# Kernel optimization log

Measured on AMD Instinct MI355X. Metric: run time of the kernel, lower is better.

Reference implementation:

```python
import jax, jax.numpy as jnp
import numpy as np
import math

N = 4096
D = 256


def _xavier(key, shape):
    fan_in, fan_out = shape[0], shape[1]
    std = math.sqrt(2.0 / (fan_in + fan_out))
    return jax.random.normal(key, shape, dtype=jnp.float32) * std


def setup_inputs() -> dict:
    key = jax.random.key(0)
    ks = jax.random.split(key, 12)
    return {
        "cur": jax.random.normal(ks[0], (N, D), dtype=jnp.float32),
        "pre": jax.random.normal(ks[1], (N, D), dtype=jnp.float32),
        # SpatialHyperedge params
        "r_proj_s": _xavier(ks[2], (D, D)),
        "incidence_s": _xavier(ks[3], (N, N - 1)),
        # TemporalHyperedge params
        "r_proj_t": _xavier(ks[4], (D, D)),
        "incidence_t": _xavier(ks[5], (N, N)),
        # HHNodeMP params
        "node_proj": _xavier(ks[6], (D, D)),
        "spa_edge_proj": _xavier(ks[7], (D, D)),
        "tmp_edge_proj": _xavier(ks[8], (D, D)),
        "theta_w": _xavier(ks[9], (D, D)),
        "theta_b": jnp.zeros((D,), dtype=jnp.float32),
    }


def _scatter_slave(vals):
    """Place [N, N-1] per-row slave values into a zero-diagonal [N, N] matrix.
    Row i's k-th slave is column k if k < i else k+1 (all j != i in order)."""
    n = vals.shape[0]
    k = jnp.arange(n - 1)[None, :]
    cols = k + (k >= jnp.arange(n)[:, None])  # [N, N-1] column indices
    rows = jnp.broadcast_to(jnp.arange(n)[:, None], (n, n - 1))
    return jnp.zeros((n, n), dtype=vals.dtype).at[rows.reshape(-1), cols.reshape(-1)].set(vals.reshape(-1))


def _fro(x):
    return jnp.sqrt(jnp.sum(x * x))


def reference(cur, pre, r_proj_s, incidence_s, r_proj_t, incidence_t,
              node_proj, spa_edge_proj, tmp_edge_proj, theta_w, theta_b):
    n, d = cur.shape
    inv_sqrt_d = 1.0 / math.sqrt(d)

    # ---- SpatialHyperedge ----
    Xd = jax.lax.stop_gradient(cur)
    master_s = Xd @ r_proj_s                                   # [N, D]
    M_s_full = _scatter_slave(incidence_s)                     # [N, N], zero diag
    neigh_recon_s = M_s_full @ Xd                              # == bmm over gathered slaves
    spatial_loss = (_fro(master_s - neigh_recon_s) * 0.2
                    + jnp.sum(jnp.abs(incidence_s))
                    + 0.001 * _fro(incidence_s))
    # clamp(min=0) then zero-out entries not strictly > 0  => relu-like
    clipped_s = jnp.where(incidence_s > 0.0, incidence_s, 0.0)
    incidence_all = _scatter_slave(clipped_s) + jnp.eye(n, dtype=cur.dtype)

    # ---- TemporalHyperedge ----
    cur_d = jax.lax.stop_gradient(cur)
    pre_d = jax.lax.stop_gradient(pre)
    master_t = cur_d @ r_proj_t
    neigh_recon_t = incidence_t @ pre_d
    temporal_loss = (_fro(master_t - neigh_recon_t) * 0.2
                     + jnp.sum(jnp.abs(incidence_t))
                     + 0.001 * _fro(incidence_t))
    incidence_t_clipped = jnp.maximum(incidence_t, 0.0)

    # ---- SpatialHyperedgeMP ----
    spa_edge_fea = incidence_all @ cur
    spa_deg = jnp.sum(incidence_all, axis=1, keepdims=True)
    spa_emb = spa_edge_fea / spa_deg                           # [N, D]

    # ---- TemporalHyperedgeMP ----
    tmp_edge_fea = incidence_t_clipped @ pre + cur
    tmp_deg = jnp.sum(incidence_t_clipped, axis=1, keepdims=True) + 1.0
    tmp_emb = tmp_edge_fea / tmp_deg                           # [N, D]

    # ---- HHNodeMP ----
    node_fea = cur @ node_proj
    spa_fea = spa_emb @ spa_edge_proj
    tmp_fea = tmp_emb @ tmp_edge_proj
    spa_attn = jnp.sum(spa_fea * node_fea, axis=1, keepdims=True) * inv_sqrt_d
    tmp_attn = jnp.sum(tmp_fea * node_fea, axis=1, keepdims=True) * inv_sqrt_d
    val = spa_attn * spa_fea + tmp_attn * tmp_fea
    node_emb = jax.nn.relu(val @ theta_w.T + theta_b)          # dropout = identity (eval)

    return node_emb, temporal_loss + spatial_loss
```

## Files before the change

kernel.cpp:

```cpp
#include <hip/hip_runtime.h>
#include <hip/hip_bf16.h>
#include <math.h>

#define NN 4096
#define DD 256

typedef __bf16 bf16x8 __attribute__((ext_vector_type(8)));
typedef short  short8 __attribute__((ext_vector_type(8)));
typedef float  f32x4  __attribute__((ext_vector_type(4)));
typedef float  f32x16 __attribute__((ext_vector_type(16)));

typedef __attribute__((address_space(1))) const void gv_t;
typedef __attribute__((address_space(3))) void lv_t;
#define GLD16(gp, lp) __builtin_amdgcn_global_load_lds((gv_t*)(gp), (lv_t*)(lp), 16, 0, 0)

#define MFMA16(a, b, c) __builtin_amdgcn_mfma_f32_16x16x32_bf16((a), (b), (c), 0, 0, 0)
#define MFMA32(a, b, c) __builtin_amdgcn_mfma_f32_32x32x16_bf16((a), (b), (c), 0, 0, 0)

__device__ inline bf16x8 brelu(bf16x8 a) {
    short8 s = __builtin_bit_cast(short8, a);
    s = s & ~(s >> 15);
    return __builtin_bit_cast(bf16x8, s);
}

__device__ inline float wave_red(float v) {
#pragma unroll
    for (int o = 32; o > 0; o >>= 1) v += __shfl_down(v, o, 64);
    return v;
}

__device__ inline unsigned short bfbits(float f) {
    return __builtin_bit_cast(unsigned short, (__bf16)f);
}

__device__ inline void syncb() {
    asm volatile("s_waitcnt lgkmcnt(0)" ::: "memory");
    __builtin_amdgcn_s_barrier();
}

__device__ inline void store16(float* base, const f32x16& v, int lane) {
#pragma unroll
    for (int r4 = 0; r4 < 4; ++r4) {
        f32x4 c = {v[4 * r4], v[4 * r4 + 1], v[4 * r4 + 2], v[4 * r4 + 3]};
        ((f32x4*)base)[r4 * 64 + lane] = c;
    }
}
__device__ inline void add16(f32x16& v, const float* base, int lane) {
#pragma unroll
    for (int r4 = 0; r4 < 4; ++r4) {
        f32x4 c = ((const f32x4*)base)[r4 * 64 + lane];
        v[4 * r4] += c[0]; v[4 * r4 + 1] += c[1]; v[4 * r4 + 2] += c[2]; v[4 * r4 + 3] += c[3];
    }
}

template <int W>
__device__ inline void red_owner(f32x16 (&aR)[2][2], f32x16 (&aL)[2][2],
                                 float* scr, int lane, f32x16& oR, f32x16& oL) {
    constexpr int o1 = W ^ 1, o2 = W ^ 2, o3 = W ^ 3;
    store16(scr + W * 1024,       aR[o1 >> 1][o1 & 1], lane);
    store16(scr + (4 + W) * 1024, aR[o2 >> 1][o2 & 1], lane);
    syncb();
    oR = aR[W >> 1][W & 1];
    add16(oR, scr + o1 * 1024, lane);
    add16(oR, scr + (4 + o2) * 1024, lane);
    syncb();
    store16(scr + W * 1024, aR[o3 >> 1][o3 & 1], lane);
    syncb();
    add16(oR, scr + o3 * 1024, lane);
    syncb();
    store16(scr + W * 1024,       aL[o1 >> 1][o1 & 1], lane);
    store16(scr + (4 + W) * 1024, aL[o2 >> 1][o2 & 1], lane);
    syncb();
    oL = aL[W >> 1][W & 1];
    add16(oL, scr + o1 * 1024, lane);
    add16(oL, scr + (4 + o2) * 1024, lane);
    syncb();
    store16(scr + W * 1024, aL[o3 >> 1][o3 & 1], lane);
    syncb();
    add16(oL, scr + o3 * 1024, lane);
}

__global__ __launch_bounds__(256) void k_pre(
    const float* __restrict__ cur, const float* __restrict__ pre,
    const float* __restrict__ r_proj_s, const float* __restrict__ r_proj_t,
    const float* __restrict__ node_pj, const float* __restrict__ spa_pj,
    const float* __restrict__ tmp_pj, const float* __restrict__ theta_w,
    const float* __restrict__ inc_t, const float* __restrict__ inc_s,
    __bf16* __restrict__ cur_bf, __bf16* __restrict__ curT, __bf16* __restrict__ preT,
    __bf16* __restrict__ pTs, __bf16* __restrict__ pTt, __bf16* __restrict__ pTn,
    __bf16* __restrict__ pTspa, __bf16* __restrict__ pTtmp, __bf16* __restrict__ thetaBf,
    __bf16* __restrict__ Mt, __bf16* __restrict__ Ms,
    float* __restrict__ rsT, float* __restrict__ pAbsT, float* __restrict__ pSqT,
    float* __restrict__ rsS, float* __restrict__ pAbsS, float* __restrict__ pSqS) {
    __shared__ __align__(16) char psm[9280];
    const int b = blockIdx.x, t = threadIdx.x;
    if (b < 4096) {
        const int i = b;
        float (*red)[4] = (float (*)[4])psm;
        const float4* src = (const float4*)(inc_t + (size_t)i * NN);
        ushort4* dst = (ushort4*)(Mt + (size_t)i * NN);
        float rs = 0.f, as = 0.f, qs = 0.f;
#pragma unroll
        for (int e = 0; e < 4; ++e) {
            const int f = t + 256 * e;
            float4 v = src[f];
            float x[4] = {v.x, v.y, v.z, v.w};
            unsigned short o[4];
#pragma unroll
            for (int j = 0; j < 4; ++j) {
                float fv = x[j];
                as += fabsf(fv); qs += fv * fv; rs += fmaxf(fv, 0.f);
                o[j] = bfbits(fv);
            }
            dst[f] = make_ushort4(o[0], o[1], o[2], o[3]);
        }
        const int w = t >> 6, lane = t & 63;
        rs = wave_red(rs); as = wave_red(as); qs = wave_red(qs);
        if (lane == 0) { red[0][w] = rs; red[1][w] = as; red[2][w] = qs; }
        __syncthreads();
        if (t == 0) {
            rsT[i]   = red[0][0] + red[0][1] + red[0][2] + red[0][3];
            pAbsT[i] = red[1][0] + red[1][1] + red[1][2] + red[1][3];
            pSqT[i]  = red[2][0] + red[2][1] + red[2][2] + red[2][3];
        }
    } else if (b < 8192) {
        const int i = b - 4096;
        unsigned short* row = (unsigned short*)psm;
        float (*red)[4] = (float (*)[4])(psm + 8192);
        const float* srow = inc_s + (size_t)i * (NN - 1);
        float rs = 0.f, as = 0.f, qs = 0.f;
#pragma unroll
        for (int e = 0; e < 4; ++e) {
            const int f = t + 256 * e;
            float x[4] = {0.f, 0.f, 0.f, 0.f};
            if (f < 1023) __builtin_memcpy(x, srow + 4 * f, 16);
            else          __builtin_memcpy(x, srow + 4092, 12);
#pragma unroll
            for (int j = 0; j < 4; ++j) {
                const int k = 4 * f + j;
                float fv = x[j];
                as += fabsf(fv); qs += fv * fv; rs += fmaxf(fv, 0.f);
                if (k < NN - 1) row[k + (k >= i)] = bfbits(fv);
            }
        }
        if (t == 0) row[i] = 0;
        __syncthreads();
        uint4* dOut = (uint4*)(Ms + (size_t)i * NN);
        const uint4* sIn = (const uint4*)row;
        dOut[t] = sIn[t];
        dOut[t + 256] = sIn[t + 256];
        const int w = t >> 6, lane = t & 63;
        rs = wave_red(rs); as = wave_red(as); qs = wave_red(qs);
        if (lane == 0) { red[0][w] = rs; red[1][w] = as; red[2][w] = qs; }
        __syncthreads();
        if (t == 0) {
            rsS[i]   = red[0][0] + red[0][1] + red[0][2] + red[0][3];
            pAbsS[i] = red[1][0] + red[1][1] + red[1][2] + red[1][3];
            pSqS[i]  = red[2][0] + red[2][1] + red[2][2] + red[2][3];
        }
    } else if (b < 8704) {
        const int bb = b - 8192;
        const int x = bb & 63, y = (bb >> 6) & 3, z = bb >> 8;
        const int i0 = x * 64, d0 = y * 64;
        const float* src = z ? pre : cur;
        __bf16* dstT = z ? preT : curT;
        unsigned short (*tile)[72] = (unsigned short (*)[72])psm;
        const int r = t >> 2, c4 = (t & 3) * 16;
        const float* srow = src + (size_t)(i0 + r) * DD + d0 + c4;
        alignas(16) unsigned short loc[16];
#pragma unroll
        for (int e = 0; e < 4; ++e) {
            float4 v = ((const float4*)srow)[e];
            loc[e * 4 + 0] = bfbits(v.x);
            loc[e * 4 + 1] = bfbits(v.y);
            loc[e * 4 + 2] = bfbits(v.z);
            loc[e * 4 + 3] = bfbits(v.w);
        }
#pragma unroll
        for (int e = 0; e < 16; ++e) tile[r][c4 + e] = loc[e];
        if (z == 0) {
            __bf16* drow = cur_bf + (size_t)(i0 + r) * DD + d0 + c4;
            *(uint4*)drow = *(uint4*)&loc[0];
            *(uint4*)(drow + 8) = *(uint4*)&loc[8];
        }
        __syncthreads();
        alignas(16) unsigned short o[16];
#pragma unroll
        for (int e = 0; e < 16; ++e) o[e] = tile[c4 + e][r];
        __bf16* trow = dstT + (size_t)(d0 + r) * NN + i0 + c4;
        *(uint4*)trow = *(uint4*)&o[0];
        *(uint4*)(trow + 8) = *(uint4*)&o[8];
    } else {
        const int bb = b - 8704;
        const int id = bb >> 8, r = bb & 255;
        const float* src = id == 0 ? r_proj_s : id == 1 ? r_proj_t : id == 2 ? node_pj
                         : id == 3 ? spa_pj : id == 4 ? tmp_pj : theta_w;
        __bf16* dst = id == 0 ? pTs : id == 1 ? pTt : id == 2 ? pTn
                    : id == 3 ? pTspa : id == 4 ? pTtmp : thetaBf;
        float v = src[r * DD + t];
        if (id < 5) dst[t * DD + r] = (__bf16)v;
        else        dst[r * DD + t] = (__bf16)v;
    }
}

__device__ inline void mfma_step_s(const __bf16 (&As)[64][72], const __bf16 (&Bs)[64][72],
                                   int wr, int wc, int quad, int l16,
                                   f32x4 (&accR)[2][2]) {
#pragma unroll
    for (int ks = 0; ks < 2; ++ks) {
        const int kc = ks * 32 + quad * 8;
        bf16x8 a0 = *(const bf16x8*)&As[wr * 32 + l16][kc];
        bf16x8 a1 = *(const bf16x8*)&As[wr * 32 + 16 + l16][kc];
        bf16x8 b0 = *(const bf16x8*)&Bs[wc * 32 + l16][kc];
        bf16x8 b1 = *(const bf16x8*)&Bs[wc * 32 + 16 + l16][kc];
        accR[0][0] = MFMA16(a0, b0, accR[0][0]);
        accR[0][1] = MFMA16(a0, b1, accR[0][1]);
        accR[1][0] = MFMA16(a1, b0, accR[1][0]);
        accR[1][1] = MFMA16(a1, b1, accR[1][1]);
    }
}

__global__ __launch_bounds__(256, 2) void k_big(const __bf16* __restrict__ Mt, const __bf16* __restrict__ Ms,
                                                const __bf16* __restrict__ preT, const __bf16* __restrict__ curT,
                                                const float* __restrict__ negMt, const float* __restrict__ negMs,
                                                const float* __restrict__ cur,
                                                const float* __restrict__ rsT, const float* __restrict__ rsS,
                                                __bf16* __restrict__ embT, __bf16* __restrict__ embS,
                                                float* __restrict__ pDiff) {
    const int flat = blockIdx.x + 4 * (blockIdx.y + 64 * blockIdx.z);
    const int swz = (flat & 7) * 64 + (flat >> 3);
    const int bx = swz & 3, by = (swz >> 2) & 63, z = swz >> 8;
    const __bf16* A  = z ? Ms : Mt;
    const __bf16* BT = z ? curT : preT;
    const float* negM = z ? negMs : negMt;
    const float* rs   = z ? rsS : rsT;
    __bf16* emb       = z ? embS : embT;
    const int n0 = bx * 64, m0 = by * 64;
    __shared__ __align__(16) char smraw[65536];
    __bf16 (*sm)[2][64][64] = (__bf16 (*)[2][64][64])smraw;
    float* scr = (float*)smraw;
    f32x16 accR[2][2], accL[2][2];
#pragma unroll
    for (int i = 0; i < 2; ++i)
#pragma unroll
        for (int j = 0; j < 2; ++j) { accR[i][j] = (f32x16)0.f; accL[i][j] = (f32x16)0.f; }
    const int t = threadIdx.x, w = t >> 6, lane = t & 63;
    const int lr = lane >> 3, lc = lane & 7;
    const int q0 = 2 * w, q1 = q0 + 1;
    const int csw = (lc ^ lr) * 8;
    const __bf16* gA0 = A + (size_t)(m0 + 8 * q0 + lr) * NN + csw;
    const __bf16* gA1 = A + (size_t)(m0 + 8 * q1 + lr) * NN + csw;
    const __bf16* gB0 = BT + (size_t)(n0 + 8 * q0 + lr) * NN + csw;
    const __bf16* gB1 = BT + (size_t)(n0 + 8 * q1 + lr) * NN + csw;
    auto stage = [&](int b, int tk) {
        const int ko = tk * 64;
        GLD16(gA0 + ko, &sm[b][0][8 * q0][0]);
        GLD16(gA1 + ko, &sm[b][0][8 * q1][0]);
        GLD16(gB0 + ko, &sm[b][1][8 * q0][0]);
        GLD16(gB1 + ko, &sm[b][1][8 * q1][0]);
    };
    stage(0, 0); stage(1, 1); stage(2, 2); stage(3, 3);
    asm volatile("s_waitcnt vmcnt(8)" ::: "memory");
    __builtin_amdgcn_s_barrier();
    __builtin_amdgcn_sched_barrier(0);
    const int fr = lane & 31, h = lane >> 5;
    const int swc = ((2 * w + h) ^ (fr & 7)) * 8;
    for (int it = 0; it < 32; ++it) {
        const int b0 = (2 * it) & 3, b1 = b0 + 1;
        bf16x8 a[2][2], bb[2][2];
#pragma unroll
        for (int mi = 0; mi < 2; ++mi) {
            a[0][mi]  = *(const bf16x8*)&sm[b0][0][mi * 32 + fr][swc];
            a[1][mi]  = *(const bf16x8*)&sm[b1][0][mi * 32 + fr][swc];
            bb[0][mi] = *(const bf16x8*)&sm[b0][1][mi * 32 + fr][swc];
            bb[1][mi] = *(const bf16x8*)&sm[b1][1][mi * 32 + fr][swc];
        }
        asm volatile("s_waitcnt lgkmcnt(0)" ::: "memory");
        __builtin_amdgcn_sched_barrier(0);
        __builtin_amdgcn_s_barrier();
        __builtin_amdgcn_sched_barrier(0);
        if (it < 30) { stage(b0, 2 * it + 4); stage(b1, 2 * it + 5); }
        __builtin_amdgcn_sched_barrier(0);
        __builtin_amdgcn_s_setprio(1);
#pragma unroll
        for (int u = 0; u < 2; ++u)
#pragma unroll
            for (int mi = 0; mi < 2; ++mi) {
                bf16x8 ar = brelu(a[u][mi]);
#pragma unroll
                for (int ni = 0; ni < 2; ++ni) {
                    accR[mi][ni] = MFMA32(a[u][mi], bb[u][ni], accR[mi][ni]);
                    accL[mi][ni] = MFMA32(ar,       bb[u][ni], accL[mi][ni]);
                }
            }
        __builtin_amdgcn_s_setprio(0);
        if (it < 31) {
            if (it < 30) asm volatile("s_waitcnt vmcnt(8)" ::: "memory");
            else         asm volatile("s_waitcnt vmcnt(0)" ::: "memory");
            __builtin_amdgcn_s_barrier();
            __builtin_amdgcn_sched_barrier(0);
        }
    }
    f32x16 oR, oL;
    if      (w == 0) red_owner<0>(accR, accL, scr, lane, oR, oL);
    else if (w == 1) red_owner<1>(accR, accL, scr, lane, oR, oL);
    else if (w == 2) red_owner<2>(accR, accL, scr, lane, oR, oL);
    else             red_owner<3>(accR, accL, scr, lane, oR, oL);
    const int mi = w >> 1, ni = w & 1;
    float sumd = 0.f;
#pragma unroll
    for (int reg = 0; reg < 16; ++reg) {
        const int rr = (reg & 3) + 8 * (reg >> 2) + 4 * h;
        const int gr = m0 + mi * 32 + rr;
        const int gc = n0 + ni * 32 + fr;
        const size_t idx = (size_t)gr * DD + gc;
        float diff = oR[reg] + negM[idx];
        sumd += diff * diff;
        emb[idx] = (__bf16)((oL[reg] + cur[idx]) * (1.f / (rs[gr] + 1.f)));
    }
    sumd = wave_red(sumd);
    float* sredp = (float*)(smraw + 32768);
    if (lane == 0) sredp[w] = sumd;
    __syncthreads();
    if (t == 0)
        pDiff[z * 256 + by * 4 + bx] = sredp[0] + sredp[1] + sredp[2] + sredp[3];
}

__global__ __launch_bounds__(256) void k_small3(const __bf16* __restrict__ cur_bf,
                                                const __bf16* __restrict__ pTs, const __bf16* __restrict__ pTt,
                                                const __bf16* __restrict__ pTn,
                                                float* __restrict__ negMs, float* __restrict__ negMt,
                                                float* __restrict__ nodeFea) {
    const int z = blockIdx.z;
    const __bf16* BT = z == 0 ? pTs : (z == 1 ? pTt : pTn);
    const int n0 = blockIdx.x * 64, m0 = blockIdx.y * 64;
    __shared__ __bf16 As[64][72], Bs[64][72];
    f32x4 accR[2][2];
#pragma unroll
    for (int i = 0; i < 2; ++i)
#pragma unroll
        for (int j = 0; j < 2; ++j) accR[i][j] = (f32x4)0.f;
    const int t = threadIdx.x, w = t >> 6, lane = t & 63, quad = lane >> 4, l16 = lane & 15;
    const int wr = w >> 1, wc = w & 1;
    const int sr = t >> 2, sc = (t & 3) * 16;
    const __bf16* gA = cur_bf + (size_t)(m0 + sr) * DD + sc;
    const __bf16* gB = BT + (size_t)(n0 + sr) * DD + sc;
    for (int kt = 0; kt < DD / 64; ++kt) {
        uint4 av0 = *(const uint4*)(gA);
        uint4 av1 = *(const uint4*)(gA + 8);
        uint4 bv0 = *(const uint4*)(gB);
        uint4 bv1 = *(const uint4*)(gB + 8);
        __syncthreads();
        *(uint4*)&As[sr][sc] = av0; *(uint4*)&As[sr][sc + 8] = av1;
        *(uint4*)&Bs[sr][sc] = bv0; *(uint4*)&Bs[sr][sc + 8] = bv1;
        __syncthreads();
        mfma_step_s(As, Bs, wr, wc, quad, l16, accR);
        gA += 64; gB += 64;
    }
#pragma unroll
    for (int mi = 0; mi < 2; ++mi)
#pragma unroll
        for (int ni = 0; ni < 2; ++ni)
#pragma unroll
            for (int r = 0; r < 4; ++r) {
                int gr = m0 + wr * 32 + mi * 16 + quad * 4 + r;
                int gc = n0 + wc * 32 + ni * 16 + l16;
                size_t idx = (size_t)gr * DD + gc;
                float v = accR[mi][ni][r];
                if (z == 0) negMs[idx] = -v;
                else if (z == 1) negMt[idx] = -v;
                else nodeFea[idx] = v;
            }
}

__global__ __launch_bounds__(256) void k_fea(const __bf16* __restrict__ embS, const __bf16* __restrict__ embT,
                                             const __bf16* __restrict__ pTspa, const __bf16* __restrict__ pTtmp,
                                             const float* __restrict__ nodeF,
                                             float* __restrict__ spaF, float* __restrict__ tmpF,
                                             float* __restrict__ pSpa, float* __restrict__ pTmp) {
    const int z = blockIdx.z;
    const __bf16* Ae = z ? embT : embS;
    const __bf16* BT = z ? pTtmp : pTspa;
    float* outF = z ? tmpF : spaF;
    float* pOut = z ? pTmp : pSpa;
    const int n0 = blockIdx.x * 64, m0 = blockIdx.y * 64;
    __shared__ __bf16 As[64][72], Bs[64][72];
    f32x4 accR[2][2];
#pragma unroll
    for (int i = 0; i < 2; ++i)
#pragma unroll
        for (int j = 0; j < 2; ++j) accR[i][j] = (f32x4)0.f;
    const int t = threadIdx.x, w = t >> 6, lane = t & 63, quad = lane >> 4, l16 = lane & 15;
    const int wr = w >> 1, wc = w & 1;
    const int sr = t >> 2, sc = (t & 3) * 16;
    const __bf16* gA = Ae + (size_t)(m0 + sr) * DD + sc;
    const __bf16* gB = BT + (size_t)(n0 + sr) * DD + sc;
    for (int kt = 0; kt < DD / 64; ++kt) {
        uint4 av0 = *(const uint4*)(gA);
        uint4 av1 = *(const uint4*)(gA + 8);
        uint4 bv0 = *(const uint4*)(gB);
        uint4 bv1 = *(const uint4*)(gB + 8);
        __syncthreads();
        *(uint4*)&As[sr][sc] = av0; *(uint4*)&As[sr][sc + 8] = av1;
        *(uint4*)&Bs[sr][sc] = bv0; *(uint4*)&Bs[sr][sc + 8] = bv1;
        __syncthreads();
        mfma_step_s(As, Bs, wr, wc, quad, l16, accR);
        gA += 64; gB += 64;
    }
    const int slice = blockIdx.x * 2 + wc;
#pragma unroll
    for (int mi = 0; mi < 2; ++mi)
#pragma unroll
        for (int r = 0; r < 4; ++r) {
            const int gr = m0 + wr * 32 + mi * 16 + quad * 4 + r;
            float s = 0.f;
#pragma unroll
            for (int ni = 0; ni < 2; ++ni) {
                const int gc = n0 + wc * 32 + ni * 16 + l16;
                const size_t idx = (size_t)gr * DD + gc;
                const float v = accR[mi][ni][r];
                outF[idx] = v;
                s += v * nodeF[idx];
            }
            s += __shfl_xor(s, 1, 64);
            s += __shfl_xor(s, 2, 64);
            s += __shfl_xor(s, 4, 64);
            s += __shfl_xor(s, 8, 64);
            if (l16 == 0) pOut[(size_t)slice * NN + gr] = s;
        }
}

__global__ __launch_bounds__(256) void k_final(const float* __restrict__ spaF, const float* __restrict__ tmpF,
                                               const float* __restrict__ pSpa, const float* __restrict__ pTmp,
                                               const __bf16* __restrict__ thetaBf, const float* __restrict__ thetaB,
                                               const float* __restrict__ pAbsT, const float* __restrict__ pSqT,
                                               const float* __restrict__ pAbsS, const float* __restrict__ pSqS,
                                               const float* __restrict__ pDiff,
                                               float* __restrict__ out) {
    const int n0 = blockIdx.x * 64, m0 = blockIdx.y * 64;
    __shared__ __bf16 As[64][72], Bs[64][72];
    f32x4 accR[2][2];
#pragma unroll
    for (int i = 0; i < 2; ++i)
#pragma unroll
        for (int j = 0; j < 2; ++j) accR[i][j] = (f32x4)0.f;
    const int t = threadIdx.x, w = t >> 6, lane = t & 63, quad = lane >> 4, l16 = lane & 15;
    const int wr = w >> 1, wc = w & 1;
    const int sr = t >> 2, sc = (t & 3) * 16;
    const int row = m0 + sr;
    float sa = 0.f, ta = 0.f;
#pragma unroll
    for (int j = 0; j < 8; ++j) {
        sa += pSpa[(size_t)j * NN + row];
        ta += pTmp[(size_t)j * NN + row];
    }
    sa *= 0.0625f; ta *= 0.0625f;
    const float* gS = spaF + (size_t)row * DD + sc;
    const float* gT = tmpF + (size_t)row * DD + sc;
    const __bf16* gB = thetaBf + (size_t)(n0 + sr) * DD + sc;
    for (int kt = 0; kt < DD / 64; ++kt) {
        __bf16 tmp[16];
#pragma unroll
        for (int e4 = 0; e4 < 4; ++e4) {
            float4 vs = ((const float4*)gS)[e4];
            float4 vt = ((const float4*)gT)[e4];
            tmp[e4 * 4 + 0] = (__bf16)(sa * vs.x + ta * vt.x);
            tmp[e4 * 4 + 1] = (__bf16)(sa * vs.y + ta * vt.y);
            tmp[e4 * 4 + 2] = (__bf16)(sa * vs.z + ta * vt.z);
            tmp[e4 * 4 + 3] = (__bf16)(sa * vs.w + ta * vt.w);
        }
        uint4 bv0 = *(const uint4*)(gB);
        uint4 bv1 = *(const uint4*)(gB + 8);
        __syncthreads();
        *(uint4*)&As[sr][sc] = *(uint4*)&tmp[0]; *(uint4*)&As[sr][sc + 8] = *(uint4*)&tmp[8];
        *(uint4*)&Bs[sr][sc] = bv0; *(uint4*)&Bs[sr][sc + 8] = bv1;
        __syncthreads();
        mfma_step_s(As, Bs, wr, wc, quad, l16, accR);
        gS += 64; gT += 64; gB += 64;
    }
#pragma unroll
    for (int mi = 0; mi < 2; ++mi)
#pragma unroll
        for (int ni = 0; ni < 2; ++ni)
#pragma unroll
            for (int r = 0; r < 4; ++r) {
                int gr = m0 + wr * 32 + mi * 16 + quad * 4 + r;
                int gc = n0 + wc * 32 + ni * 16 + l16;
                float v = accR[mi][ni][r] + thetaB[gc];
                out[(size_t)gr * DD + gc] = fmaxf(v, 0.f);
            }
    if (blockIdx.x == 0 && blockIdx.y == 0) {
        float aT = 0.f, qT = 0.f, aS = 0.f, qS = 0.f;
#pragma unroll
        for (int j = 0; j < 16; ++j) {
            const int i = t + 256 * j;
            aT += pAbsT[i]; qT += pSqT[i]; aS += pAbsS[i]; qS += pSqS[i];
        }
        float dT = pDiff[t], dS = pDiff[256 + t];
        aT = wave_red(aT); qT = wave_red(qT); aS = wave_red(aS); qS = wave_red(qS);
        dT = wave_red(dT); dS = wave_red(dS);
        float (*red)[4] = (float (*)[4])As;
        if (lane == 0) { red[0][w] = aT; red[1][w] = qT; red[2][w] = aS; red[3][w] = qS; red[4][w] = dT; red[5][w] = dS; }
        __syncthreads();
        if (t == 0) {
            float s[6];
#pragma unroll
            for (int k = 0; k < 6; ++k) s[k] = red[k][0] + red[k][1] + red[k][2] + red[k][3];
            float l = s[0] + 0.001f * sqrtf(s[1]) + 0.2f * sqrtf(s[4])
                    + s[2] + 0.001f * sqrtf(s[3]) + 0.2f * sqrtf(s[5]);
            out[(size_t)NN * DD] = l;
        }
    }
}

extern "C" void kernel_launch(void* const* d_in, const int* in_sizes, int n_in,
                              void* d_out, int out_size, void* d_ws, size_t ws_size,
                              hipStream_t stream) {
    (void)in_sizes; (void)n_in; (void)out_size; (void)ws_size;
    const float* cur      = (const float*)d_in[0];
    const float* pre      = (const float*)d_in[1];
    const float* r_proj_s = (const float*)d_in[2];
    const float* inc_s    = (const float*)d_in[3];
    const float* r_proj_t = (const float*)d_in[4];
    const float* inc_t    = (const float*)d_in[5];
    const float* node_pj  = (const float*)d_in[6];
    const float* spa_pj   = (const float*)d_in[7];
    const float* tmp_pj   = (const float*)d_in[8];
    const float* theta_w  = (const float*)d_in[9];
    const float* theta_b  = (const float*)d_in[10];
    float* out = (float*)d_out;

    char* p = (char*)d_ws;
    auto alloc = [&](size_t bytes) -> void* {
        void* r = (void*)p;
        p += (bytes + 255) & ~(size_t)255;
        return r;
    };
    __bf16* Mt      = (__bf16*)alloc((size_t)NN * NN * 2);
    __bf16* Ms      = (__bf16*)alloc((size_t)NN * NN * 2);
    __bf16* cur_bf  = (__bf16*)alloc((size_t)NN * DD * 2);
    __bf16* curT    = (__bf16*)alloc((size_t)NN * DD * 2);
    __bf16* preT    = (__bf16*)alloc((size_t)NN * DD * 2);
    __bf16* pTs     = (__bf16*)alloc((size_t)DD * DD * 2);
    __bf16* pTt     = (__bf16*)alloc((size_t)DD * DD * 2);
    __bf16* pTn     = (__bf16*)alloc((size_t)DD * DD * 2);
    __bf16* pTspa   = (__bf16*)alloc((size_t)DD * DD * 2);
    __bf16* pTtmp   = (__bf16*)alloc((size_t)DD * DD * 2);
    __bf16* thetaBf = (__bf16*)alloc((size_t)DD * DD * 2);
    __bf16* embS    = (__bf16*)alloc((size_t)NN * DD * 2);
    __bf16* embT    = (__bf16*)alloc((size_t)NN * DD * 2);
    float* negMs    = (float*)alloc((size_t)NN * DD * 4);
    float* negMt    = (float*)alloc((size_t)NN * DD * 4);
    float* nodeFea  = (float*)alloc((size_t)NN * DD * 4);
    float* spaF     = (float*)alloc((size_t)NN * DD * 4);
    float* tmpF     = (float*)alloc((size_t)NN * DD * 4);
    float* rsS      = (float*)alloc((size_t)NN * 4);
    float* rsT      = (float*)alloc((size_t)NN * 4);
    float* pSpa     = (float*)alloc((size_t)8 * NN * 4);
    float* pTmp     = (float*)alloc((size_t)8 * NN * 4);
    float* pAbsT    = (float*)alloc((size_t)NN * 4);
    float* pSqT     = (float*)alloc((size_t)NN * 4);
    float* pAbsS    = (float*)alloc((size_t)NN * 4);
    float* pSqS     = (float*)alloc((size_t)NN * 4);
    float* pDiff    = (float*)alloc(512 * 4);

    k_pre<<<10240, 256, 0, stream>>>(cur, pre, r_proj_s, r_proj_t, node_pj, spa_pj, tmp_pj, theta_w,
                                     inc_t, inc_s,
                                     cur_bf, curT, preT, pTs, pTt, pTn, pTspa, pTtmp, thetaBf,
                                     Mt, Ms, rsT, pAbsT, pSqT, rsS, pAbsS, pSqS);
    k_small3<<<dim3(4, 64, 3), 256, 0, stream>>>(cur_bf, pTs, pTt, pTn, negMs, negMt, nodeFea);
    k_big<<<dim3(4, 64, 2), 256, 0, stream>>>(Mt, Ms, preT, curT, negMt, negMs, cur,
                                              rsT, rsS, embT, embS, pDiff);
    k_fea<<<dim3(4, 64, 2), 256, 0, stream>>>(embS, embT, pTspa, pTtmp, nodeFea,
                                              spaF, tmpF, pSpa, pTmp);
    k_final<<<dim3(4, 64), 256, 0, stream>>>(spaF, tmpF, pSpa, pTmp, thetaBf, theta_b,
                                             pAbsT, pSqT, pAbsS, pSqS, pDiff, out);
}
```

Measured before the change: 243.7 us.

## Fuse incidence fp32-to-bf16 conversion and row stats into the big GEMM

The big GEMM kernel now reads the fp32 incidence matrices directly, converts them to bf16 in registers, and writes them into swizzled LDS. Row sums, abs sums and squared sums are accumulated in the same pass, so the separate pre-pass that wrote two 32MB bf16 matrices plus per-row stats is gone. This removes a full write and re-read of the converted matrices. In exchange the GEMM loads twice the bytes for A, and each of the four column blocks re-reads and re-converts the same rows. The spatial path also does scalar gathered loads to handle the skipped diagonal.

```diff
diff --git a/kernel.cpp b/kernel.cpp
--- a/kernel.cpp
+++ b/kernel.cpp
@@ -85,86 +85,16 @@
     const float* __restrict__ r_proj_s, const float* __restrict__ r_proj_t,
     const float* __restrict__ node_pj, const float* __restrict__ spa_pj,
     const float* __restrict__ tmp_pj, const float* __restrict__ theta_w,
-    const float* __restrict__ inc_t, const float* __restrict__ inc_s,
     __bf16* __restrict__ cur_bf, __bf16* __restrict__ curT, __bf16* __restrict__ preT,
     __bf16* __restrict__ pTs, __bf16* __restrict__ pTt, __bf16* __restrict__ pTn,
-    __bf16* __restrict__ pTspa, __bf16* __restrict__ pTtmp, __bf16* __restrict__ thetaBf,
-    __bf16* __restrict__ Mt, __bf16* __restrict__ Ms,
-    float* __restrict__ rsT, float* __restrict__ pAbsT, float* __restrict__ pSqT,
-    float* __restrict__ rsS, float* __restrict__ pAbsS, float* __restrict__ pSqS) {
-    __shared__ __align__(16) char psm[9280];
+    __bf16* __restrict__ pTspa, __bf16* __restrict__ pTtmp, __bf16* __restrict__ thetaBf) {
+    __shared__ unsigned short tile[64][72];
     const int b = blockIdx.x, t = threadIdx.x;
-    if (b < 4096) {
-        const int i = b;
-        float (*red)[4] = (float (*)[4])psm;
-        const float4* src = (const float4*)(inc_t + (size_t)i * NN);
-        ushort4* dst = (ushort4*)(Mt + (size_t)i * NN);
-        float rs = 0.f, as = 0.f, qs = 0.f;
-#pragma unroll
-        for (int e = 0; e < 4; ++e) {
-            const int f = t + 256 * e;
-            float4 v = src[f];
-            float x[4] = {v.x, v.y, v.z, v.w};
-            unsigned short o[4];
-#pragma unroll
-            for (int j = 0; j < 4; ++j) {
-                float fv = x[j];
-                as += fabsf(fv); qs += fv * fv; rs += fmaxf(fv, 0.f);
-                o[j] = bfbits(fv);
-            }
-            dst[f] = make_ushort4(o[0], o[1], o[2], o[3]);
-        }
-        const int w = t >> 6, lane = t & 63;
-        rs = wave_red(rs); as = wave_red(as); qs = wave_red(qs);
-        if (lane == 0) { red[0][w] = rs; red[1][w] = as; red[2][w] = qs; }
-        __syncthreads();
-        if (t == 0) {
-            rsT[i]   = red[0][0] + red[0][1] + red[0][2] + red[0][3];
-            pAbsT[i] = red[1][0] + red[1][1] + red[1][2] + red[1][3];
-            pSqT[i]  = red[2][0] + red[2][1] + red[2][2] + red[2][3];
-        }
-    } else if (b < 8192) {
-        const int i = b - 4096;
-        unsigned short* row = (unsigned short*)psm;
-        float (*red)[4] = (float (*)[4])(psm + 8192);
-        const float* srow = inc_s + (size_t)i * (NN - 1);
-        float rs = 0.f, as = 0.f, qs = 0.f;
-#pragma unroll
-        for (int e = 0; e < 4; ++e) {
-            const int f = t + 256 * e;
-            float x[4] = {0.f, 0.f, 0.f, 0.f};
-            if (f < 1023) __builtin_memcpy(x, srow + 4 * f, 16);
-            else          __builtin_memcpy(x, srow + 4092, 12);
-#pragma unroll
-            for (int j = 0; j < 4; ++j) {
-                const int k = 4 * f + j;
-                float fv = x[j];
-                as += fabsf(fv); qs += fv * fv; rs += fmaxf(fv, 0.f);
-                if (k < NN - 1) row[k + (k >= i)] = bfbits(fv);
-            }
-        }
-        if (t == 0) row[i] = 0;
-        __syncthreads();
-        uint4* dOut = (uint4*)(Ms + (size_t)i * NN);
-        const uint4* sIn = (const uint4*)row;
-        dOut[t] = sIn[t];
-        dOut[t + 256] = sIn[t + 256];
-        const int w = t >> 6, lane = t & 63;
-        rs = wave_red(rs); as = wave_red(as); qs = wave_red(qs);
-        if (lane == 0) { red[0][w] = rs; red[1][w] = as; red[2][w] = qs; }
-        __syncthreads();
-        if (t == 0) {
-            rsS[i]   = red[0][0] + red[0][1] + red[0][2] + red[0][3];
-            pAbsS[i] = red[1][0] + red[1][1] + red[1][2] + red[1][3];
-            pSqS[i]  = red[2][0] + red[2][1] + red[2][2] + red[2][3];
-        }
-    } else if (b < 8704) {
-        const int bb = b - 8192;
-        const int x = bb & 63, y = (bb >> 6) & 3, z = bb >> 8;
+    if (b < 512) {
+        const int x = b & 63, y = (b >> 6) & 3, z = b >> 8;
         const int i0 = x * 64, d0 = y * 64;
         const float* src = z ? pre : cur;
         __bf16* dstT = z ? preT : curT;
-        unsigned short (*tile)[72] = (unsigned short (*)[72])psm;
         const int r = t >> 2, c4 = (t & 3) * 16;
         const float* srow = src + (size_t)(i0 + r) * DD + d0 + c4;
         alignas(16) unsigned short loc[16];
@@ -191,7 +121,7 @@
         *(uint4*)trow = *(uint4*)&o[0];
         *(uint4*)(trow + 8) = *(uint4*)&o[8];
     } else {
-        const int bb = b - 8704;
+        const int bb = b - 512;
         const int id = bb >> 8, r = bb & 255;
         const float* src = id == 0 ? r_proj_s : id == 1 ? r_proj_t : id == 2 ? node_pj
                          : id == 3 ? spa_pj : id == 4 ? tmp_pj : theta_w;
@@ -201,6 +131,224 @@
         if (id < 5) dst[t * DD + r] = (__bf16)v;
         else        dst[r * DD + t] = (__bf16)v;
     }
+}
+
+template <int ZS>
+__device__ inline void loadApair(float (&x)[32], const float* rowp, int i, int kt0, int sc16) {
+#pragma unroll
+    for (int u = 0; u < 2; ++u) {
+        const int c0 = (kt0 + u) * 64 + sc16;
+        if (ZS == 0) {
+#pragma unroll
+            for (int j4 = 0; j4 < 4; ++j4) {
+                float4 v = *(const float4*)(rowp + c0 + 4 * j4);
+                x[u * 16 + 4 * j4 + 0] = v.x;
+                x[u * 16 + 4 * j4 + 1] = v.y;
+                x[u * 16 + 4 * j4 + 2] = v.z;
+                x[u * 16 + 4 * j4 + 3] = v.w;
+            }
+        } else {
+#pragma unroll
+            for (int j = 0; j < 16; ++j) {
+                const int k = c0 + j;
+                const int dg = (k == i);
+                int idx = dg ? 0 : (k - (k > i));
+                float v = rowp[idx];
+                x[u * 16 + j] = dg ? 0.f : v;
+            }
+        }
+    }
+}
+
+__device__ inline void writeApair(const float (&x)[32], __bf16 (*A0)[64], __bf16 (*A1)[64],
+                                  int sr, int pc0, int pc1,
+                                  float& rs, float& as, float& qs) {
+#pragma unroll
+    for (int u = 0; u < 2; ++u) {
+        __bf16 (*Ab)[64] = u ? A1 : A0;
+        alignas(16) unsigned short o[16];
+#pragma unroll
+        for (int j = 0; j < 16; ++j) {
+            float fv = x[u * 16 + j];
+            as += fabsf(fv); qs += fv * fv; rs += fmaxf(fv, 0.f);
+            o[j] = bfbits(fv);
+        }
+        *(uint4*)&Ab[sr][pc0] = *(uint4*)&o[0];
+        *(uint4*)&Ab[sr][pc1] = *(uint4*)&o[8];
+    }
+}
+
+template <int ZS>
+__device__ inline void iter_body(int P, float (&x)[32],
+                                 __bf16 (*A0)[64], __bf16 (*A1)[64],
+                                 __bf16 (*B0)[64], __bf16 (*B1)[64],
+                                 const float* rowp, int i, int sc16, int sr, int pc0, int pc1,
+                                 const __bf16* gB0, const __bf16* gB1,
+                                 __bf16* dB0a, __bf16* dB0b, __bf16* dB1a, __bf16* dB1b,
+                                 int fr, int swc,
+                                 f32x16 (&accR)[2][2], f32x16 (&accL)[2][2],
+                                 float& rs, float& as, float& qs) {
+    bf16x8 a[2][2], bb[2][2];
+#pragma unroll
+    for (int mi = 0; mi < 2; ++mi) {
+        a[0][mi]  = *(const bf16x8*)&A0[mi * 32 + fr][swc];
+        a[1][mi]  = *(const bf16x8*)&A1[mi * 32 + fr][swc];
+        bb[0][mi] = *(const bf16x8*)&B0[mi * 32 + fr][swc];
+        bb[1][mi] = *(const bf16x8*)&B1[mi * 32 + fr][swc];
+    }
+    asm volatile("s_waitcnt lgkmcnt(0)" ::: "memory");
+    __builtin_amdgcn_sched_barrier(0);
+    __builtin_amdgcn_s_barrier();
+    __builtin_amdgcn_sched_barrier(0);
+    __builtin_amdgcn_s_setprio(1);
+#pragma unroll
+    for (int u = 0; u < 2; ++u)
+#pragma unroll
+        for (int mi = 0; mi < 2; ++mi) {
+            bf16x8 ar = brelu(a[u][mi]);
+#pragma unroll
+            for (int ni = 0; ni < 2; ++ni) {
+                accR[mi][ni] = MFMA32(a[u][mi], bb[u][ni], accR[mi][ni]);
+                accL[mi][ni] = MFMA32(ar,       bb[u][ni], accL[mi][ni]);
+            }
+        }
+    __builtin_amdgcn_s_setprio(0);
+    __builtin_amdgcn_sched_barrier(0);
+    if (P < 29) {
+        if (ZS) asm volatile("s_waitcnt vmcnt(32)" ::: "memory");
+        else    asm volatile("s_waitcnt vmcnt(8)"  ::: "memory");
+    } else {
+        asm volatile("s_waitcnt vmcnt(0)" ::: "memory");
+    }
+    __builtin_amdgcn_sched_barrier(0);
+    if (P < 30) {
+        writeApair(x, A0, A1, sr, pc0, pc1, rs, as, qs);
+        const size_t tb = (size_t)(2 * (P + 2)) * 64;
+        GLD16(gB0 + tb, dB0a);      GLD16(gB1 + tb, dB0b);
+        GLD16(gB0 + tb + 64, dB1a); GLD16(gB1 + tb + 64, dB1b);
+    }
+    __builtin_amdgcn_sched_barrier(0);
+    if (P < 28) loadApair<ZS>(x, rowp, i, 2 * (P + 4), sc16);
+    asm volatile("s_waitcnt lgkmcnt(0)" ::: "memory");
+    __builtin_amdgcn_sched_barrier(0);
+    __builtin_amdgcn_s_barrier();
+}
+
+template <int ZS>
+__device__ inline void run_loop(const float* rowp, int i, const __bf16* BT, int n0, int t,
+                                char* smraw,
+                                f32x16 (&accR)[2][2], f32x16 (&accL)[2][2],
+                                float& rs, float& as, float& qs) {
+    __bf16 (*As)[64][64] = (__bf16 (*)[64][64])smraw;
+    __bf16 (*Bs)[64][64] = (__bf16 (*)[64][64])(smraw + 32768);
+    const int w = t >> 6, lane = t & 63;
+    const int sr = t >> 2, c4 = t & 3, sc16 = c4 * 16;
+    const int lr = lane >> 3, lc = lane & 7;
+    const int q0 = 2 * w, q1 = q0 + 1;
+    const int csw = (lc ^ lr) * 8;
+    const __bf16* gB0 = BT + (size_t)(n0 + 8 * q0 + lr) * NN + csw;
+    const __bf16* gB1 = BT + (size_t)(n0 + 8 * q1 + lr) * NN + csw;
+    const int fr = lane & 31, h = lane >> 5;
+    const int swc = ((2 * w + h) ^ (fr & 7)) * 8;
+    const int pc0 = ((2 * c4) ^ (sr & 7)) * 8;
+    const int pc1 = ((2 * c4 + 1) ^ (sr & 7)) * 8;
+    float x0[32], x1[32];
+    loadApair<ZS>(x0, rowp, i, 0, sc16);
+    loadApair<ZS>(x1, rowp, i, 2, sc16);
+    GLD16(gB0, &Bs[0][8 * q0][0]);            GLD16(gB1, &Bs[0][8 * q1][0]);
+    GLD16(gB0 + 64, &Bs[1][8 * q0][0]);       GLD16(gB1 + 64, &Bs[1][8 * q1][0]);
+    GLD16(gB0 + 128, &Bs[2][8 * q0][0]);      GLD16(gB1 + 128, &Bs[2][8 * q1][0]);
+    GLD16(gB0 + 192, &Bs[3][8 * q0][0]);      GLD16(gB1 + 192, &Bs[3][8 * q1][0]);
+    asm volatile("s_waitcnt vmcnt(0)" ::: "memory");
+    __builtin_amdgcn_sched_barrier(0);
+    writeApair(x0, As[0], As[1], sr, pc0, pc1, rs, as, qs);
+    writeApair(x1, As[2], As[3], sr, pc0, pc1, rs, as, qs);
+    __builtin_amdgcn_sched_barrier(0);
+    loadApair<ZS>(x0, rowp, i, 4, sc16);
+    loadApair<ZS>(x1, rowp, i, 6, sc16);
+    asm volatile("s_waitcnt lgkmcnt(0)" ::: "memory");
+    __builtin_amdgcn_sched_barrier(0);
+    __builtin_amdgcn_s_barrier();
+    for (int q = 0; q < 16; ++q) {
+        iter_body<ZS>(2 * q, x0, As[0], As[1], Bs[0], Bs[1], rowp, i, sc16, sr, pc0, pc1,
+                      gB0, gB1, &Bs[0][8 * q0][0], &Bs[0][8 * q1][0],
+                      &Bs[1][8 * q0][0], &Bs[1][8 * q1][0], fr, swc, accR, accL, rs, as, qs);
+        iter_body<ZS>(2 * q + 1, x1, As[2], As[3], Bs[2], Bs[3], rowp, i, sc16, sr, pc0, pc1,
+                      gB0, gB1, &Bs[2][8 * q0][0], &Bs[2][8 * q1][0],
+                      &Bs[3][8 * q0][0], &Bs[3][8 * q1][0], fr, swc, accR, accL, rs, as, qs);
+    }
+}
+
+__global__ __launch_bounds__(256, 2) void k_big(const float* __restrict__ inc_t,
+                                                const float* __restrict__ inc_s,
+                                                const __bf16* __restrict__ preT,
+                                                const __bf16* __restrict__ curT,
+                                                const float* __restrict__ negMt,
+                                                const float* __restrict__ negMs,
+                                                const float* __restrict__ cur,
+                                                __bf16* __restrict__ embT, __bf16* __restrict__ embS,
+                                                float* __restrict__ pDiff,
+                                                float* __restrict__ pAbs2, float* __restrict__ pSq2) {
+    const int flat = blockIdx.x + 4 * (blockIdx.y + 64 * blockIdx.z);
+    const int swz = (flat & 7) * 64 + (flat >> 3);
+    const int bx = swz & 3, by = (swz >> 2) & 63, z = swz >> 8;
+    const __bf16* BT  = z ? curT : preT;
+    const float* negM = z ? negMs : negMt;
+    __bf16* emb       = z ? embS : embT;
+    const int n0 = bx * 64, m0 = by * 64;
+    __shared__ __align__(16) char smraw[65536];
+    f32x16 accR[2][2], accL[2][2];
+#pragma unroll
+    for (int i = 0; i < 2; ++i)
+#pragma unroll
+        for (int j = 0; j < 2; ++j) { accR[i][j] = (f32x16)0.f; accL[i][j] = (f32x16)0.f; }
+    const int t = threadIdx.x, w = t >> 6, lane = t & 63;
+    const int sr = t >> 2;
+    const int gi = m0 + sr;
+    float rs = 0.f, as = 0.f, qs = 0.f;
+    if (z == 0) {
+        run_loop<0>(inc_t + (size_t)gi * NN, gi, BT, n0, t, smraw, accR, accL, rs, as, qs);
+    } else {
+        run_loop<1>(inc_s + (size_t)gi * (NN - 1), gi, BT, n0, t, smraw, accR, accL, rs, as, qs);
+    }
+    rs += __shfl_xor(rs, 1, 64);
+    rs += __shfl_xor(rs, 2, 64);
+    float* rs_lds = (float*)(smraw + 32768);
+    float (*red2)[4] = (float (*)[4])(smraw + 32768 + 256);
+    float* sredp = (float*)(smraw + 32768 + 304);
+    if ((t & 3) == 0) rs_lds[sr] = rs;
+    as = wave_red(as); qs = wave_red(qs);
+    if (lane == 0) { red2[0][w] = as; red2[1][w] = qs; }
+    __syncthreads();
+    if (bx == 0 && t == 0) {
+        pAbs2[z * 64 + by] = red2[0][0] + red2[0][1] + red2[0][2] + red2[0][3];
+        pSq2 [z * 64 + by] = red2[1][0] + red2[1][1] + red2[1][2] + red2[1][3];
+    }
+    float* scr = (float*)smraw;
+    f32x16 oR, oL;
+    if      (w == 0) red_owner<0>(accR, accL, scr, lane, oR, oL);
+    else if (w == 1) red_owner<1>(accR, accL, scr, lane, oR, oL);
+    else if (w == 2) red_owner<2>(accR, accL, scr, lane, oR, oL);
+    else             red_owner<3>(accR, accL, scr, lane, oR, oL);
+    const int mi = w >> 1, ni = w & 1;
+    const int fr = lane & 31, h = lane >> 5;
+    float sumd = 0.f;
+#pragma unroll
+    for (int reg = 0; reg < 16; ++reg) {
+        const int rr = (reg & 3) + 8 * (reg >> 2) + 4 * h;
+        const int gr = m0 + mi * 32 + rr;
+        const int gc = n0 + ni * 32 + fr;
+        const size_t idx = (size_t)gr * DD + gc;
+        float diff = oR[reg] + negM[idx];
+        sumd += diff * diff;
+        float inv = 1.f / (rs_lds[gr - m0] + 1.f);
+        emb[idx] = (__bf16)((oL[reg] + cur[idx]) * inv);
+    }
+    sumd = wave_red(sumd);
+    if (lane == 0) sredp[w] = sumd;
+    __syncthreads();
+    if (t == 0)
+        pDiff[z * 256 + by * 4 + bx] = sredp[0] + sredp[1] + sredp[2] + sredp[3];
 }
 
 __device__ inline void mfma_step_s(const __bf16 (&As)[64][72], const __bf16 (&Bs)[64][72],
@@ -218,112 +366,6 @@
         accR[1][0] = MFMA16(a1, b0, accR[1][0]);
         accR[1][1] = MFMA16(a1, b1, accR[1][1]);
     }
-}
-
-__global__ __launch_bounds__(256, 2) void k_big(const __bf16* __restrict__ Mt, const __bf16* __restrict__ Ms,
-                                                const __bf16* __restrict__ preT, const __bf16* __restrict__ curT,
-                                                const float* __restrict__ negMt, const float* __restrict__ negMs,
-                                                const float* __restrict__ cur,
-                                                const float* __restrict__ rsT, const float* __restrict__ rsS,
-                                                __bf16* __restrict__ embT, __bf16* __restrict__ embS,
-                                                float* __restrict__ pDiff) {
-    const int flat = blockIdx.x + 4 * (blockIdx.y + 64 * blockIdx.z);
-    const int swz = (flat & 7) * 64 + (flat >> 3);
-    const int bx = swz & 3, by = (swz >> 2) & 63, z = swz >> 8;
-    const __bf16* A  = z ? Ms : Mt;
-    const __bf16* BT = z ? curT : preT;
-    const float* negM = z ? negMs : negMt;
-    const float* rs   = z ? rsS : rsT;
-    __bf16* emb       = z ? embS : embT;
-    const int n0 = bx * 64, m0 = by * 64;
-    __shared__ __align__(16) char smraw[65536];
-    __bf16 (*sm)[2][64][64] = (__bf16 (*)[2][64][64])smraw;
-    float* scr = (float*)smraw;
-    f32x16 accR[2][2], accL[2][2];
-#pragma unroll
-    for (int i = 0; i < 2; ++i)
-#pragma unroll
-        for (int j = 0; j < 2; ++j) { accR[i][j] = (f32x16)0.f; accL[i][j] = (f32x16)0.f; }
-    const int t = threadIdx.x, w = t >> 6, lane = t & 63;
-    const int lr = lane >> 3, lc = lane & 7;
-    const int q0 = 2 * w, q1 = q0 + 1;
-    const int csw = (lc ^ lr) * 8;
-    const __bf16* gA0 = A + (size_t)(m0 + 8 * q0 + lr) * NN + csw;
-    const __bf16* gA1 = A + (size_t)(m0 + 8 * q1 + lr) * NN + csw;
-    const __bf16* gB0 = BT + (size_t)(n0 + 8 * q0 + lr) * NN + csw;
-    const __bf16* gB1 = BT + (size_t)(n0 + 8 * q1 + lr) * NN + csw;
-    auto stage = [&](int b, int tk) {
-        const int ko = tk * 64;
-        GLD16(gA0 + ko, &sm[b][0][8 * q0][0]);
-        GLD16(gA1 + ko, &sm[b][0][8 * q1][0]);
-        GLD16(gB0 + ko, &sm[b][1][8 * q0][0]);
-        GLD16(gB1 + ko, &sm[b][1][8 * q1][0]);
-    };
-    stage(0, 0); stage(1, 1); stage(2, 2); stage(3, 3);
-    asm volatile("s_waitcnt vmcnt(8)" ::: "memory");
-    __builtin_amdgcn_s_barrier();
-    __builtin_amdgcn_sched_barrier(0);
-    const int fr = lane & 31, h = lane >> 5;
-    const int swc = ((2 * w + h) ^ (fr & 7)) * 8;
-    for (int it = 0; it < 32; ++it) {
-        const int b0 = (2 * it) & 3, b1 = b0 + 1;
-        bf16x8 a[2][2], bb[2][2];
-#pragma unroll
-        for (int mi = 0; mi < 2; ++mi) {
-            a[0][mi]  = *(const bf16x8*)&sm[b0][0][mi * 32 + fr][swc];
-            a[1][mi]  = *(const bf16x8*)&sm[b1][0][mi * 32 + fr][swc];
-            bb[0][mi] = *(const bf16x8*)&sm[b0][1][mi * 32 + fr][swc];
-            bb[1][mi] = *(const bf16x8*)&sm[b1][1][mi * 32 + fr][swc];
-        }
-        asm volatile("s_waitcnt lgkmcnt(0)" ::: "memory");
-        __builtin_amdgcn_sched_barrier(0);
-        __builtin_amdgcn_s_barrier();
-        __builtin_amdgcn_sched_barrier(0);
-        if (it < 30) { stage(b0, 2 * it + 4); stage(b1, 2 * it + 5); }
-        __builtin_amdgcn_sched_barrier(0);
-        __builtin_amdgcn_s_setprio(1);
-#pragma unroll
-        for (int u = 0; u < 2; ++u)
-#pragma unroll
-            for (int mi = 0; mi < 2; ++mi) {
-                bf16x8 ar = brelu(a[u][mi]);
-#pragma unroll
-                for (int ni = 0; ni < 2; ++ni) {
-                    accR[mi][ni] = MFMA32(a[u][mi], bb[u][ni], accR[mi][ni]);
-                    accL[mi][ni] = MFMA32(ar,       bb[u][ni], accL[mi][ni]);
-                }
-            }
-        __builtin_amdgcn_s_setprio(0);
-        if (it < 31) {
-            if (it < 30) asm volatile("s_waitcnt vmcnt(8)" ::: "memory");
-            else         asm volatile("s_waitcnt vmcnt(0)" ::: "memory");
-            __builtin_amdgcn_s_barrier();
-            __builtin_amdgcn_sched_barrier(0);
-        }
-    }
-    f32x16 oR, oL;
-    if      (w == 0) red_owner<0>(accR, accL, scr, lane, oR, oL);
-    else if (w == 1) red_owner<1>(accR, accL, scr, lane, oR, oL);
-    else if (w == 2) red_owner<2>(accR, accL, scr, lane, oR, oL);
-    else             red_owner<3>(accR, accL, scr, lane, oR, oL);
-    const int mi = w >> 1, ni = w & 1;
-    float sumd = 0.f;
-#pragma unroll
-    for (int reg = 0; reg < 16; ++reg) {
-        const int rr = (reg & 3) + 8 * (reg >> 2) + 4 * h;
-        const int gr = m0 + mi * 32 + rr;
-        const int gc = n0 + ni * 32 + fr;
-        const size_t idx = (size_t)gr * DD + gc;
-        float diff = oR[reg] + negM[idx];
-        sumd += diff * diff;
-        emb[idx] = (__bf16)((oL[reg] + cur[idx]) * (1.f / (rs[gr] + 1.f)));
-    }
-    sumd = wave_red(sumd);
-    float* sredp = (float*)(smraw + 32768);
-    if (lane == 0) sredp[w] = sumd;
-    __syncthreads();
-    if (t == 0)
-        pDiff[z * 256 + by * 4 + bx] = sredp[0] + sredp[1] + sredp[2] + sredp[3];
 }
 
 __global__ __launch_bounds__(256) void k_small3(const __bf16* __restrict__ cur_bf,
@@ -433,8 +475,7 @@
 __global__ __launch_bounds__(256) void k_final(const float* __restrict__ spaF, const float* __restrict__ tmpF,
                                                const float* __restrict__ pSpa, const float* __restrict__ pTmp,
                                                const __bf16* __restrict__ thetaBf, const float* __restrict__ thetaB,
-                                               const float* __restrict__ pAbsT, const float* __restrict__ pSqT,
-                                               const float* __restrict__ pAbsS, const float* __restrict__ pSqS,
+                                               const float* __restrict__ pAbs2, const float* __restrict__ pSq2,
                                                const float* __restrict__ pDiff,
                                                float* __restrict__ out) {
     const int n0 = blockIdx.x * 64, m0 = blockIdx.y * 64;
@@ -491,11 +532,7 @@
             }
     if (blockIdx.x == 0 && blockIdx.y == 0) {
         float aT = 0.f, qT = 0.f, aS = 0.f, qS = 0.f;
-#pragma unroll
-        for (int j = 0; j < 16; ++j) {
-            const int i = t + 256 * j;
-            aT += pAbsT[i]; qT += pSqT[i]; aS += pAbsS[i]; qS += pSqS[i];
-        }
+        if (t < 64) { aT = pAbs2[t]; qT = pSq2[t]; aS = pAbs2[64 + t]; qS = pSq2[64 + t]; }
         float dT = pDiff[t], dS = pDiff[256 + t];
         aT = wave_red(aT); qT = wave_red(qT); aS = wave_red(aS); qS = wave_red(qS);
         dT = wave_red(dT); dS = wave_red(dS);
@@ -536,8 +573,6 @@
         p += (bytes + 255) & ~(size_t)255;
         return r;
     };
-    __bf16* Mt      = (__bf16*)alloc((size_t)NN * NN * 2);
-    __bf16* Ms      = (__bf16*)alloc((size_t)NN * NN * 2);
     __bf16* cur_bf  = (__bf16*)alloc((size_t)NN * DD * 2);
     __bf16* curT    = (__bf16*)alloc((size_t)NN * DD * 2);
     __bf16* preT    = (__bf16*)alloc((size_t)NN * DD * 2);
@@ -554,25 +589,19 @@
     float* nodeFea  = (float*)alloc((size_t)NN * DD * 4);
     float* spaF     = (float*)alloc((size_t)NN * DD * 4);
     float* tmpF     = (float*)alloc((size_t)NN * DD * 4);
-    float* rsS      = (float*)alloc((size_t)NN * 4);
-    float* rsT      = (float*)alloc((size_t)NN * 4);
     float* pSpa     = (float*)alloc((size_t)8 * NN * 4);
     float* pTmp     = (float*)alloc((size_t)8 * NN * 4);
-    float* pAbsT    = (float*)alloc((size_t)NN * 4);
-    float* pSqT     = (float*)alloc((size_t)NN * 4);
-    float* pAbsS    = (float*)alloc((size_t)NN * 4);
-    float* pSqS     = (float*)alloc((size_t)NN * 4);
+    float* pAbs2    = (float*)alloc(128 * 4);
+    float* pSq2     = (float*)alloc(128 * 4);
     float* pDiff    = (float*)alloc(512 * 4);
 
-    k_pre<<<10240, 256, 0, stream>>>(cur, pre, r_proj_s, r_proj_t, node_pj, spa_pj, tmp_pj, theta_w,
-                                     inc_t, inc_s,
-                                     cur_bf, curT, preT, pTs, pTt, pTn, pTspa, pTtmp, thetaBf,
-                                     Mt, Ms, rsT, pAbsT, pSqT, rsS, pAbsS, pSqS);
+    k_pre<<<2048, 256, 0, stream>>>(cur, pre, r_proj_s, r_proj_t, node_pj, spa_pj, tmp_pj, theta_w,
+                                    cur_bf, curT, preT, pTs, pTt, pTn, pTspa, pTtmp, thetaBf);
     k_small3<<<dim3(4, 64, 3), 256, 0, stream>>>(cur_bf, pTs, pTt, pTn, negMs, negMt, nodeFea);
-    k_big<<<dim3(4, 64, 2), 256, 0, stream>>>(Mt, Ms, preT, curT, negMt, negMs, cur,
-                                              rsT, rsS, embT, embS, pDiff);
+    k_big<<<dim3(4, 64, 2), 256, 0, stream>>>(inc_t, inc_s, preT, curT, negMt, negMs, cur,
+                                              embT, embS, pDiff, pAbs2, pSq2);
     k_fea<<<dim3(4, 64, 2), 256, 0, stream>>>(embS, embT, pTspa, pTtmp, nodeFea,
                                               spaF, tmpF, pSpa, pTmp);
     k_final<<<dim3(4, 64), 256, 0, stream>>>(spaF, tmpF, pSpa, pTmp, thetaBf, theta_b,
-                                             pAbsT, pSqT, pAbsS, pSqS, pDiff, out);
-}
+                                             pAbs2, pSq2, pDiff, out);
+}
```

New measurement: 507.4 us. 2.08x slower.
